# Optimization experiments

Measured on AMD Instinct MI355X. Metric: run time of the kernel, lower is better.

Reference implementation:

```python
import jax, jax.numpy as jnp
import numpy as np

N_HEAD = 8
EPS_LN = 1e-5
EPS_SM = 1e-16


def _mlp(x, w1, b1, g, beta, w2, b2):
    # Linear -> ReLU -> LayerNorm -> Linear (matches nn.Sequential in torch module)
    h = jax.nn.relu(x @ w1 + b1)
    mu = jnp.mean(h, axis=-1, keepdims=True)
    var = jnp.mean((h - mu) ** 2, axis=-1, keepdims=True)
    h = (h - mu) * jax.lax.rsqrt(var + EPS_LN) * g + beta
    return h @ w2 + b2


def setup_inputs() -> dict:
    B, L, D, E, Fe, H = 4, 4096, 128, 262144, 5, N_HEAD
    ks = jax.random.split(jax.random.key(0), 20)
    s = 0.02
    p = lambda i, sh: jax.random.normal(ks[i], sh, jnp.float32) * s
    z = lambda n: jnp.zeros((n,), jnp.float32)
    inp = {
        "key": jax.random.normal(ks[0], (B, L, D), jnp.float32),
        "value": jax.random.normal(ks[1], (B, L, D), jnp.float32),
        "query": jax.random.normal(ks[2], (B, L, D), jnp.float32),
        "edge_feats": jax.random.normal(ks[3], (E, Fe), jnp.float32),
        "atten_masks": jnp.zeros((E,), jnp.float32),  # present in signature, unused in forward
        "batch_indices": jax.random.randint(ks[4], (E,), 0, B),
        "head_indices": jax.random.randint(ks[5], (E,), 0, L),
        "tail_indices": jax.random.randint(ks[6], (E,), 0, L),
        "key_w": p(7, (D, D)), "key_b": z(D),
        "query_w": p(8, (D, D)), "query_b": z(D),
        "value_w": p(9, (D, D)), "value_b": z(D),
        "proj_w": p(10, (D, D)), "proj_b": z(D),
        "ea_w1": p(11, (Fe, D)), "ea_b1": z(D), "ea_g": jnp.ones((D,), jnp.float32), "ea_beta": z(D), "ea_w2": p(12, (D, H)), "ea_b2": z(H),
        "ek_w1": p(13, (Fe, D)), "ek_b1": z(D), "ek_g": jnp.ones((D,), jnp.float32), "ek_beta": z(D), "ek_w2": p(14, (D, D)), "ek_b2": z(D),
        "ev_w1": p(15, (Fe, D)), "ev_b1": z(D), "ev_g": jnp.ones((D,), jnp.float32), "ev_beta": z(D), "ev_w2": p(16, (D, D)), "ev_b2": z(D),
    }
    return inp


def reference(key, value, query, edge_feats, atten_masks,
              batch_indices, head_indices, tail_indices,
              key_w, key_b, query_w, query_b, value_w, value_b, proj_w, proj_b,
              ea_w1, ea_b1, ea_g, ea_beta, ea_w2, ea_b2,
              ek_w1, ek_b1, ek_g, ek_beta, ek_w2, ek_b2,
              ev_w1, ev_b1, ev_g, ev_beta, ev_w2, ev_b2):
    B, L, D = query.shape
    H = N_HEAD
    dh = D // H
    N = B * L
    # node projections -> [B*L, H, dh]
    k = (key @ key_w + key_b).reshape(N, H, dh)
    q = (query @ query_w + query_b).reshape(N, H, dh)
    v = (value @ value_w + value_b).reshape(N, H, dh)
    heads = batch_indices * L + head_indices  # destination node per edge
    tails = batch_indices * L + tail_indices  # source node per edge
    # per-edge gather + edge-conditioned k/v
    qs = q[heads]
    ks = k[tails] + _mlp(edge_feats, ek_w1, ek_b1, ek_g, ek_beta, ek_w2, ek_b2).reshape(-1, H, dh)
    vs = v[tails] + _mlp(edge_feats, ev_w1, ev_b1, ev_g, ev_beta, ev_w2, ev_b2).reshape(-1, H, dh)
    w = jnp.sum(ks * qs, axis=-1) + _mlp(edge_feats, ea_w1, ea_b1, ea_g, ea_beta, ea_w2, ea_b2)  # [E, H]
    # segment softmax over edges grouped by destination node
    m = jax.ops.segment_max(w, heads, num_segments=N)
    ex = jnp.exp(w - m[heads])
    denom = jax.ops.segment_sum(ex, heads, num_segments=N)
    att = ex / (denom[heads] + EPS_SM)  # [E, H]
    # weighted scatter-sum combine
    y = jax.ops.segment_sum(att[:, :, None] * vs, heads, num_segments=N).reshape(B, L, D)
    return y @ proj_w + proj_b
```

## Files before the change

### kernel.cpp

```cpp
#include <hip/hip_runtime.h>
#include <hip/hip_bf16.h>

#define D      128
#define NHEAD  8
#define FE     5
#define LSEQ   4096
#define EPB    64
#define NNODE  16384
#define EPS_LN 1e-5f
#define EPS_SM 1e-16f

typedef unsigned short ushort_t;
typedef __bf16 bf16x8 __attribute__((ext_vector_type(8)));
typedef float  f32x4  __attribute__((ext_vector_type(4)));

__device__ __forceinline__ ushort_t f2bf(float x) {
    __hip_bfloat16 b = __float2bfloat16(x);
    return __builtin_bit_cast(unsigned short, b);
}
__device__ __forceinline__ float bf2f(ushort_t u) {
    __hip_bfloat16 b = __builtin_bit_cast(__hip_bfloat16, u);
    return __bfloat162float(b);
}
__device__ __forceinline__ float i2f(int x)  { return __builtin_bit_cast(float, x); }
__device__ __forceinline__ int   f2i(float x){ return __builtin_bit_cast(int, x); }

union Pk8 { ushort_t u[8]; uint4 v; };

__global__ __launch_bounds__(256) void setup_kernel(
    const float* __restrict__ key, const float* __restrict__ value,
    const float* __restrict__ query,
    const float* __restrict__ key_w, const float* __restrict__ key_b,
    const float* __restrict__ value_w, const float* __restrict__ value_b,
    const float* __restrict__ query_w, const float* __restrict__ query_b,
    ushort_t* __restrict__ k16, ushort_t* __restrict__ v16, ushort_t* __restrict__ q16,
    const float* __restrict__ ekw2, const float* __restrict__ evw2,
    const float* __restrict__ eaw2,
    ushort_t* __restrict__ eksw, ushort_t* __restrict__ evsw, ushort_t* __restrict__ easw,
    const int* __restrict__ bidx, const int* __restrict__ hidx,
    int* __restrict__ cnt, int nqb, int E)
{
    const int t  = threadIdx.x;
    const int nq = 3 * nqb;

    if ((int)blockIdx.x < nq) {
        __shared__ float xs[2][D][20];
        const int which = blockIdx.x / nqb;
        const int r0    = (blockIdx.x % nqb) * 32;
        const float* X = (which == 0) ? key   : (which == 1) ? value   : query;
        const float* W = (which == 0) ? key_w : (which == 1) ? value_w : query_w;
        const float* bias = (which == 0) ? key_b : (which == 1) ? value_b : query_b;
        ushort_t* Y = (which == 0) ? k16 : (which == 1) ? v16 : q16;

        const int rg = t >> 7, j = t & 127;
        const int rbase = r0 + rg * 16;
        {
            float tmp[16];
            #pragma unroll
            for (int r = 0; r < 16; ++r) tmp[r] = X[(size_t)(rbase + r) * D + j];
            #pragma unroll
            for (int c = 0; c < 4; ++c)
                *(float4*)&xs[rg][j][c * 4] = float4{tmp[c*4], tmp[c*4+1], tmp[c*4+2], tmp[c*4+3]};
        }
        __syncthreads();
        float acc[16];
        const float b = bias[j];
        #pragma unroll
        for (int r = 0; r < 16; ++r) acc[r] = b;
        #pragma unroll 4
        for (int i = 0; i < D; ++i) {
            const float w = W[i * D + j];
            #pragma unroll
            for (int c = 0; c < 4; ++c) {
                const float4 x4 = *(const float4*)&xs[rg][i][c * 4];
                acc[c*4+0] = fmaf(x4.x, w, acc[c*4+0]);
                acc[c*4+1] = fmaf(x4.y, w, acc[c*4+1]);
                acc[c*4+2] = fmaf(x4.z, w, acc[c*4+2]);
                acc[c*4+3] = fmaf(x4.w, w, acc[c*4+3]);
            }
        }
        #pragma unroll
        for (int r = 0; r < 16; ++r) Y[(size_t)(rbase + r) * D + j] = f2bf(acc[r]);
        return;
    }

    const int b2 = blockIdx.x - nq;
    if (b2 < 17) {
        const int g = b2 * 256 + t;
        const float* src; ushort_t* dst; int frag, ncols, nvalid;
        if (g < 2048)      { src = ekw2; dst = eksw; frag = g;        ncols = 128; nvalid = 128; }
        else if (g < 4096) { src = evw2; dst = evsw; frag = g - 2048; ncols = 128; nvalid = 128; }
        else if (g < 4352) { src = eaw2; dst = easw; frag = g - 4096; ncols = 8;   nvalid = 8; }
        else return;
        const int s = (frag >> 6) & 3;
        const int l = frag & 63;
        const int n = ((frag >> 8) << 4) + (l & 15);
        Pk8 pk;
        #pragma unroll
        for (int j = 0; j < 8; ++j) {
            const int k = s * 32 + (l >> 4) * 8 + j;
            const float v = (n < nvalid) ? src[k * ncols + n] : 0.f;
            pk.u[j] = f2bf(v);
        }
        *(uint4*)(dst + (size_t)frag * 8) = pk.v;
        return;
    }

    const int e = (b2 - 17) * 256 + t;
    if (e < E) atomicAdd(&cnt[bidx[e] * LSEQ + hidx[e]], 1);
}

__global__ __launch_bounds__(1024) void scan16k(
    const int* __restrict__ cnt, int* __restrict__ base)
{
    __shared__ int part[1024];
    const int t = threadIdx.x;
    int v[16], ex[16], s = 0;
    #pragma unroll
    for (int i = 0; i < 16; ++i) v[i] = cnt[t * 16 + i];
    #pragma unroll
    for (int i = 0; i < 16; ++i) { ex[i] = s; s += v[i]; }
    part[t] = s;
    __syncthreads();
    for (int off = 1; off < 1024; off <<= 1) {
        const int x = (t >= off) ? part[t - off] : 0;
        __syncthreads();
        part[t] += x;
        __syncthreads();
    }
    const int boff = (t > 0) ? part[t - 1] : 0;
    #pragma unroll
    for (int i = 0; i < 16; ++i) base[t * 16 + i] = boff + ex[i];
    if (t == 1023) base[NNODE] = boff + s;
}

__global__ __launch_bounds__(256) void scatter_rec(
    const int* __restrict__ bidx, const int* __restrict__ hidx, const int* __restrict__ tidx,
    const float* __restrict__ edge_feats,
    const int* __restrict__ base, int* __restrict__ cnt,
    float* __restrict__ rec, int E)
{
    const int e = blockIdx.x * 256 + threadIdx.x;
    if (e >= E) return;
    const int bb = bidx[e];
    const int nh = bb * LSEQ + hidx[e];
    const int nt = bb * LSEQ + tidx[e];
    const int slot = atomicSub(&cnt[nh], 1) - 1;
    const int p = base[nh] + slot;
    float ef[FE];
    #pragma unroll
    for (int f = 0; f < FE; ++f) ef[f] = edge_feats[(size_t)e * FE + f];
    *(float4*)&rec[(size_t)p * 8]     = float4{ef[0], ef[1], ef[2], ef[3]};
    *(float4*)&rec[(size_t)p * 8 + 4] = float4{ef[4], i2f(nh), i2f(nt), 0.f};
}

__global__ __launch_bounds__(256, 4) void edge_kernel(
    const float* __restrict__ rec,
    const float* __restrict__ ea_w1, const float* __restrict__ ea_b1,
    const float* __restrict__ ea_g,  const float* __restrict__ ea_be, const float* __restrict__ ea_b2,
    const float* __restrict__ ek_w1, const float* __restrict__ ek_b1,
    const float* __restrict__ ek_g,  const float* __restrict__ ek_be, const float* __restrict__ ek_b2,
    const float* __restrict__ ev_w1, const float* __restrict__ ev_b1,
    const float* __restrict__ ev_g,  const float* __restrict__ ev_be, const float* __restrict__ ev_b2,
    const ushort_t* __restrict__ easw, const ushort_t* __restrict__ eksw, const ushort_t* __restrict__ evsw,
    const ushort_t* __restrict__ k16, const ushort_t* __restrict__ q16, const ushort_t* __restrict__ v16,
    float* __restrict__ ex_ws, ushort_t* __restrict__ vs_ws)
{
    __shared__ float pw1[3][FE * D];
    __shared__ float pb1[3][D], pg[3][D], pbe[3][D];
    __shared__ float pb2k[D], pb2v[D], pb2a[NHEAD];
    __shared__ float ef_s[EPB][FE];
    __shared__ int   eh_s[EPB], et_s[EPB];

    const int t   = threadIdx.x;
    const int e0g = blockIdx.x * EPB;

    for (int i = t; i < FE * D; i += 256) { pw1[0][i] = ea_w1[i]; pw1[1][i] = ek_w1[i]; pw1[2][i] = ev_w1[i]; }
    if (t < D) {
        pb1[0][t] = ea_b1[t]; pb1[1][t] = ek_b1[t]; pb1[2][t] = ev_b1[t];
        pg [0][t] = ea_g [t]; pg [1][t] = ek_g [t]; pg [2][t] = ev_g [t];
        pbe[0][t] = ea_be[t]; pbe[1][t] = ek_be[t]; pbe[2][t] = ev_be[t];
        pb2k[t] = ek_b2[t];   pb2v[t] = ev_b2[t];
        if (t < NHEAD) pb2a[t] = ea_b2[t];
    }
    if (t < 128) {
        const int pl = t >> 1, half = t & 1;
        const float4 v = *(const float4*)&rec[((size_t)e0g + pl) * 8 + half * 4];
        if (half == 0) {
            ef_s[pl][0] = v.x; ef_s[pl][1] = v.y; ef_s[pl][2] = v.z; ef_s[pl][3] = v.w;
        } else {
            ef_s[pl][4] = v.x; eh_s[pl] = f2i(v.y); et_s[pl] = f2i(v.z);
        }
    }
    __syncthreads();

    const int mt   = t >> 6;
    const int l    = t & 63;
    const int qt   = l & 3;
    const int per  = l >> 2;
    const int row0 = (l >> 4) * 4;
    const int colb = l & 15;
    const int src  = 4 * colb + (l >> 4);
    const int bsrc = (l & 48);

    int tn[4], hnn[4];
    #pragma unroll
    for (int r = 0; r < 4; ++r) { tn[r] = et_s[mt*16 + row0 + r]; hnn[r] = eh_s[mt*16 + row0 + r]; }

    float efr[FE];
    #pragma unroll
    for (int f = 0; f < FE; ++f) efr[f] = ef_s[mt*16 + per][f];

    auto first_layer = [&](int m, uint4 pk[4]) {
        const float4* w1v = (const float4*)&pw1[m][0];
        const float4* b1v = (const float4*)&pb1[m][0];
        const float4* gv  = (const float4*)&pg[m][0];
        const float4* bev = (const float4*)&pbe[m][0];
        float4 hv[4][2];
        float s1 = 0.f, s2 = 0.f;
        #pragma unroll
        for (int s = 0; s < 4; ++s) {
            #pragma unroll
            for (int hc = 0; hc < 2; ++hc) {
                const int idx = s * 8 + qt * 2 + hc;
                float4 a = b1v[idx];
                #pragma unroll
                for (int f = 0; f < FE; ++f) {
                    const float sc = efr[f];
                    const float4 w = w1v[f * 32 + idx];
                    a.x = fmaf(sc, w.x, a.x); a.y = fmaf(sc, w.y, a.y);
                    a.z = fmaf(sc, w.z, a.z); a.w = fmaf(sc, w.w, a.w);
                }
                a.x = fmaxf(a.x, 0.f); a.y = fmaxf(a.y, 0.f);
                a.z = fmaxf(a.z, 0.f); a.w = fmaxf(a.w, 0.f);
                hv[s][hc] = a;
                s1 += a.x + a.y + a.z + a.w;
                s2 += a.x*a.x + a.y*a.y + a.z*a.z + a.w*a.w;
            }
        }
        s1 += __shfl_xor(s1, 1); s1 += __shfl_xor(s1, 2);
        s2 += __shfl_xor(s2, 1); s2 += __shfl_xor(s2, 2);
        const float mu = s1 * (1.f / 128.f);
        const float rs = rsqrtf(s2 * (1.f / 128.f) - mu * mu + EPS_LN);
        #pragma unroll
        for (int s = 0; s < 4; ++s) {
            const int idx = s * 8 + qt * 2;
            const float4 x0 = hv[s][0], x1 = hv[s][1];
            const float4 g0 = gv[idx], g1 = gv[idx + 1];
            const float4 b0 = bev[idx], b1 = bev[idx + 1];
            Pk8 p8;
            p8.u[0] = f2bf(fmaf((x0.x - mu) * rs, g0.x, b0.x));
            p8.u[1] = f2bf(fmaf((x0.y - mu) * rs, g0.y, b0.y));
            p8.u[2] = f2bf(fmaf((x0.z - mu) * rs, g0.z, b0.z));
            p8.u[3] = f2bf(fmaf((x0.w - mu) * rs, g0.w, b0.w));
            p8.u[4] = f2bf(fmaf((x1.x - mu) * rs, g1.x, b1.x));
            p8.u[5] = f2bf(fmaf((x1.y - mu) * rs, g1.y, b1.y));
            p8.u[6] = f2bf(fmaf((x1.z - mu) * rs, g1.z, b1.z));
            p8.u[7] = f2bf(fmaf((x1.w - mu) * rs, g1.w, b1.w));
            pk[s] = p8.v;
        }
    };

    auto gather_afr = [&](const uint4 pk[4], bf16x8 afr[4]) {
        #pragma unroll
        for (int s = 0; s < 4; ++s) {
            uint4 w;
            w.x = (unsigned)__shfl((int)pk[s].x, src);
            w.y = (unsigned)__shfl((int)pk[s].y, src);
            w.z = (unsigned)__shfl((int)pk[s].z, src);
            w.w = (unsigned)__shfl((int)pk[s].w, src);
            afr[s] = __builtin_bit_cast(bf16x8, w);
        }
    };

    uint4 pk[4];
    bf16x8 afr[4];

    float eaacc[4];
    first_layer(0, pk);
    gather_afr(pk, afr);
    {
        f32x4 acc = {0.f, 0.f, 0.f, 0.f};
        #pragma unroll
        for (int s = 0; s < 4; ++s) {
            const bf16x8 bfr = *(const bf16x8*)(easw + (size_t)(s * 64 + l) * 8);
            acc = __builtin_amdgcn_mfma_f32_16x16x32_bf16(afr[s], bfr, acc, 0, 0, 0);
        }
        #pragma unroll
        for (int r = 0; r < 4; ++r) eaacc[r] = acc[r];
    }

    first_layer(1, pk);
    gather_afr(pk, afr);
    #pragma unroll
    for (int nt = 0; nt < NHEAD; ++nt) {
        f32x4 acc = {0.f, 0.f, 0.f, 0.f};
        #pragma unroll
        for (int s = 0; s < 4; ++s) {
            const bf16x8 bfr = *(const bf16x8*)(eksw + (size_t)((nt * 4 + s) * 64 + l) * 8);
            acc = __builtin_amdgcn_mfma_f32_16x16x32_bf16(afr[s], bfr, acc, 0, 0, 0);
        }
        const int col = nt * 16 + colb;
        const float b2 = pb2k[col];
        const float ba = pb2a[nt];
        float pr[4];
        #pragma unroll
        for (int r = 0; r < 4; ++r)
            pr[r] = (acc[r] + b2 + bf2f(k16[(size_t)tn[r] * D + col]))
                    * bf2f(q16[(size_t)hnn[r] * D + col]);
        #pragma unroll
        for (int m = 1; m < 16; m <<= 1) {
            #pragma unroll
            for (int r = 0; r < 4; ++r) pr[r] += __shfl_xor(pr[r], m);
        }
        #pragma unroll
        for (int r = 0; r < 4; ++r) {
            const float ea = __shfl(eaacc[r], bsrc | nt);
            const float ex = __expf(pr[r] + ea + ba);
            if (colb == nt)
                ex_ws[(size_t)(e0g + mt*16 + row0 + r) * NHEAD + nt] = ex;
        }
    }

    first_layer(2, pk);
    gather_afr(pk, afr);
    #pragma unroll
    for (int nt = 0; nt < NHEAD; ++nt) {
        f32x4 acc = {0.f, 0.f, 0.f, 0.f};
        #pragma unroll
        for (int s = 0; s < 4; ++s) {
            const bf16x8 bfr = *(const bf16x8*)(evsw + (size_t)((nt * 4 + s) * 64 + l) * 8);
            acc = __builtin_amdgcn_mfma_f32_16x16x32_bf16(afr[s], bfr, acc, 0, 0, 0);
        }
        const int col = nt * 16 + colb;
        const float b2 = pb2v[col];
        #pragma unroll
        for (int r = 0; r < 4; ++r) {
            const float vs = acc[r] + b2 + bf2f(v16[(size_t)tn[r] * D + col]);
            vs_ws[(size_t)(e0g + mt*16 + row0 + r) * D + col] = f2bf(vs);
        }
    }
}

__global__ __launch_bounds__(512) void agg_out(
    const int* __restrict__ base,
    const float* __restrict__ ex_ws, const ushort_t* __restrict__ vs_ws,
    const float* __restrict__ W, const float* __restrict__ bias,
    float* __restrict__ out)
{
    __shared__ float xs[D][20];
    const int t  = threadIdx.x;
    const int rg = t >> 7;
    const int j  = t & 127;
    const int h  = j >> 4;
    const int n0 = blockIdx.x * 16;

    #pragma unroll
    for (int ni = 0; ni < 4; ++ni) {
        const int n  = n0 + rg * 4 + ni;
        const int s0 = base[n], s1 = base[n + 1];
        float acc = 0.f, den = 0.f;
        int p = s0;
        for (; p + 4 <= s1; p += 4) {
            float ex4[4], vs4[4];
            #pragma unroll
            for (int r = 0; r < 4; ++r) {
                ex4[r] = ex_ws[(size_t)(p + r) * NHEAD + h];
                vs4[r] = bf2f(vs_ws[(size_t)(p + r) * D + j]);
            }
            #pragma unroll
            for (int r = 0; r < 4; ++r) {
                den += ex4[r];
                acc = fmaf(ex4[r], vs4[r], acc);
            }
        }
        for (; p < s1; ++p) {
            const float ex = ex_ws[(size_t)p * NHEAD + h];
            den += ex;
            acc = fmaf(ex, bf2f(vs_ws[(size_t)p * D + j]), acc);
        }
        xs[j][rg * 4 + ni] = acc / (den + EPS_SM);
    }
    __syncthreads();

    float acc[4];
    const float b = bias[j];
    #pragma unroll
    for (int r = 0; r < 4; ++r) acc[r] = b;
    #pragma unroll 4
    for (int i = 0; i < D; ++i) {
        const float w = W[i * D + j];
        const float4 y4 = *(const float4*)&xs[i][rg * 4];
        acc[0] = fmaf(y4.x, w, acc[0]); acc[1] = fmaf(y4.y, w, acc[1]);
        acc[2] = fmaf(y4.z, w, acc[2]); acc[3] = fmaf(y4.w, w, acc[3]);
    }
    #pragma unroll
    for (int r = 0; r < 4; ++r)
        out[(size_t)(n0 + rg * 4 + r) * D + j] = acc[r];
}

extern "C" void kernel_launch(void* const* d_in, const int* in_sizes, int n_in,
                              void* d_out, int out_size, void* d_ws, size_t ws_size,
                              hipStream_t stream)
{
    const float* key        = (const float*)d_in[0];
    const float* value      = (const float*)d_in[1];
    const float* query      = (const float*)d_in[2];
    const float* edge_feats = (const float*)d_in[3];
    const int*   bidx       = (const int*)d_in[5];
    const int*   hidx       = (const int*)d_in[6];
    const int*   tidx       = (const int*)d_in[7];
    const float* key_w   = (const float*)d_in[8];  const float* key_b   = (const float*)d_in[9];
    const float* query_w = (const float*)d_in[10]; const float* query_b = (const float*)d_in[11];
    const float* value_w = (const float*)d_in[12]; const float* value_b = (const float*)d_in[13];
    const float* proj_w  = (const float*)d_in[14]; const float* proj_b  = (const float*)d_in[15];

    const int N = in_sizes[0] / D;
    const int E = in_sizes[5];

    char* ws = (char*)d_ws;
    ushort_t* k16   = (ushort_t*)ws; ws += (size_t)N * D * 2;
    ushort_t* q16   = (ushort_t*)ws; ws += (size_t)N * D * 2;
    ushort_t* v16   = (ushort_t*)ws; ws += (size_t)N * D * 2;
    float* ex_ws    = (float*)ws;    ws += (size_t)E * NHEAD * 4;
    ushort_t* vs_ws = (ushort_t*)ws; ws += (size_t)E * D * 2;
    float* rec      = (float*)ws;    ws += (size_t)E * 8 * 4;
    ushort_t* eksw  = (ushort_t*)ws; ws += (size_t)2048 * 8 * 2;
    ushort_t* evsw  = (ushort_t*)ws; ws += (size_t)2048 * 8 * 2;
    ushort_t* easw  = (ushort_t*)ws; ws += (size_t)256 * 8 * 2;
    int* base = (int*)ws;  ws += (size_t)(N + 1) * 4;
    int* cnt  = (int*)ws;  ws += (size_t)N * 4;

    const int nqb   = N / 32;
    const int nhist = (E + 255) / 256;
    const int ngrid = 3 * nqb + 17 + nhist;

    hipMemsetAsync(cnt, 0, (size_t)N * 4, stream);

    setup_kernel<<<ngrid, 256, 0, stream>>>(
        key, value, query,
        key_w, key_b, value_w, value_b, query_w, query_b,
        k16, v16, q16,
        (const float*)d_in[26], (const float*)d_in[32], (const float*)d_in[20],
        eksw, evsw, easw,
        bidx, hidx, cnt, nqb, E);

    scan16k<<<1, 1024, 0, stream>>>(cnt, base);

    scatter_rec<<<(E + 255) / 256, 256, 0, stream>>>(
        bidx, hidx, tidx, edge_feats, base, cnt, rec, E);

    edge_kernel<<<E / EPB, 256, 0, stream>>>(
        rec,
        (const float*)d_in[16], (const float*)d_in[17], (const float*)d_in[18],
        (const float*)d_in[19], (const float*)d_in[21],
        (const float*)d_in[22], (const float*)d_in[23], (const float*)d_in[24],
        (const float*)d_in[25], (const float*)d_in[27],
        (const float*)d_in[28], (const float*)d_in[29], (const float*)d_in[30],
        (const float*)d_in[31], (const float*)d_in[33],
        easw, eksw, evsw,
        k16, q16, v16,
        ex_ws, vs_ws);

    agg_out<<<N / 16, 512, 0, stream>>>(base, ex_ws, vs_ws, proj_w, proj_b, (float*)d_out);
}
```

Measured before the change: 311.4 us.

## Move K/Q/V projections to bf16 MFMA and merge them with edge scatter kernel

The fp32 FMA node projections for key/query/value are replaced by bf16 MFMA 16x16x32 tiles. Their weights are pre-swizzled into fragment layout in the pre-kernel, next to the edge MLP weights. The projection blocks move into the same launch as the edge record scatter, so the projections overlap with the scatter work and the histogram/scan runs before them. This cuts fp32 ALU cost, but inputs are now rounded to bf16 before the matmul, which lowers precision.

Result: faster. 293.5 us (-5.7%).

```diff
diff --git a/kernel.cpp b/kernel.cpp
--- a/kernel.cpp
+++ b/kernel.cpp
@@ -27,70 +27,26 @@
 
 union Pk8 { ushort_t u[8]; uint4 v; };
 
-__global__ __launch_bounds__(256) void setup_kernel(
-    const float* __restrict__ key, const float* __restrict__ value,
-    const float* __restrict__ query,
-    const float* __restrict__ key_w, const float* __restrict__ key_b,
-    const float* __restrict__ value_w, const float* __restrict__ value_b,
-    const float* __restrict__ query_w, const float* __restrict__ query_b,
-    ushort_t* __restrict__ k16, ushort_t* __restrict__ v16, ushort_t* __restrict__ q16,
+__global__ __launch_bounds__(256) void pre_kernel(
     const float* __restrict__ ekw2, const float* __restrict__ evw2,
     const float* __restrict__ eaw2,
+    const float* __restrict__ kw, const float* __restrict__ qw,
+    const float* __restrict__ vw,
     ushort_t* __restrict__ eksw, ushort_t* __restrict__ evsw, ushort_t* __restrict__ easw,
+    ushort_t* __restrict__ kwsw, ushort_t* __restrict__ qwsw, ushort_t* __restrict__ vwsw,
     const int* __restrict__ bidx, const int* __restrict__ hidx,
-    int* __restrict__ cnt, int nqb, int E)
-{
-    const int t  = threadIdx.x;
-    const int nq = 3 * nqb;
-
-    if ((int)blockIdx.x < nq) {
-        __shared__ float xs[2][D][20];
-        const int which = blockIdx.x / nqb;
-        const int r0    = (blockIdx.x % nqb) * 32;
-        const float* X = (which == 0) ? key   : (which == 1) ? value   : query;
-        const float* W = (which == 0) ? key_w : (which == 1) ? value_w : query_w;
-        const float* bias = (which == 0) ? key_b : (which == 1) ? value_b : query_b;
-        ushort_t* Y = (which == 0) ? k16 : (which == 1) ? v16 : q16;
-
-        const int rg = t >> 7, j = t & 127;
-        const int rbase = r0 + rg * 16;
-        {
-            float tmp[16];
-            #pragma unroll
-            for (int r = 0; r < 16; ++r) tmp[r] = X[(size_t)(rbase + r) * D + j];
-            #pragma unroll
-            for (int c = 0; c < 4; ++c)
-                *(float4*)&xs[rg][j][c * 4] = float4{tmp[c*4], tmp[c*4+1], tmp[c*4+2], tmp[c*4+3]};
-        }
-        __syncthreads();
-        float acc[16];
-        const float b = bias[j];
-        #pragma unroll
-        for (int r = 0; r < 16; ++r) acc[r] = b;
-        #pragma unroll 4
-        for (int i = 0; i < D; ++i) {
-            const float w = W[i * D + j];
-            #pragma unroll
-            for (int c = 0; c < 4; ++c) {
-                const float4 x4 = *(const float4*)&xs[rg][i][c * 4];
-                acc[c*4+0] = fmaf(x4.x, w, acc[c*4+0]);
-                acc[c*4+1] = fmaf(x4.y, w, acc[c*4+1]);
-                acc[c*4+2] = fmaf(x4.z, w, acc[c*4+2]);
-                acc[c*4+3] = fmaf(x4.w, w, acc[c*4+3]);
-            }
-        }
-        #pragma unroll
-        for (int r = 0; r < 16; ++r) Y[(size_t)(rbase + r) * D + j] = f2bf(acc[r]);
-        return;
-    }
-
-    const int b2 = blockIdx.x - nq;
-    if (b2 < 17) {
-        const int g = b2 * 256 + t;
-        const float* src; ushort_t* dst; int frag, ncols, nvalid;
-        if (g < 2048)      { src = ekw2; dst = eksw; frag = g;        ncols = 128; nvalid = 128; }
-        else if (g < 4096) { src = evw2; dst = evsw; frag = g - 2048; ncols = 128; nvalid = 128; }
-        else if (g < 4352) { src = eaw2; dst = easw; frag = g - 4096; ncols = 8;   nvalid = 8; }
+    int* __restrict__ cnt, int E)
+{
+    const int t = threadIdx.x;
+    if (blockIdx.x < 41) {
+        const int g = blockIdx.x * 256 + t;
+        const float* src; ushort_t* dst; int frag, ncols = 128, nvalid = 128;
+        if (g < 2048)       { src = ekw2; dst = eksw; frag = g; }
+        else if (g < 4096)  { src = evw2; dst = evsw; frag = g - 2048; }
+        else if (g < 4352)  { src = eaw2; dst = easw; frag = g - 4096; ncols = 8; nvalid = 8; }
+        else if (g < 6400)  { src = kw;   dst = kwsw; frag = g - 4352; }
+        else if (g < 8448)  { src = qw;   dst = qwsw; frag = g - 6400; }
+        else if (g < 10496) { src = vw;   dst = vwsw; frag = g - 8448; }
         else return;
         const int s = (frag >> 6) & 3;
         const int l = frag & 63;
@@ -105,8 +61,7 @@
         *(uint4*)(dst + (size_t)frag * 8) = pk.v;
         return;
     }
-
-    const int e = (b2 - 17) * 256 + t;
+    const int e = (blockIdx.x - 41) * 256 + t;
     if (e < E) atomicAdd(&cnt[bidx[e] * LSEQ + hidx[e]], 1);
 }
 
@@ -134,13 +89,67 @@
     if (t == 1023) base[NNODE] = boff + s;
 }
 
-__global__ __launch_bounds__(256) void scatter_rec(
+__global__ __launch_bounds__(256) void mid_kernel(
+    const float* __restrict__ key, const float* __restrict__ value,
+    const float* __restrict__ query,
+    const float* __restrict__ key_b, const float* __restrict__ value_b,
+    const float* __restrict__ query_b,
+    const ushort_t* __restrict__ kwsw, const ushort_t* __restrict__ vwsw,
+    const ushort_t* __restrict__ qwsw,
+    ushort_t* __restrict__ k16, ushort_t* __restrict__ v16, ushort_t* __restrict__ q16,
     const int* __restrict__ bidx, const int* __restrict__ hidx, const int* __restrict__ tidx,
     const float* __restrict__ edge_feats,
-    const int* __restrict__ base, int* __restrict__ cnt,
-    float* __restrict__ rec, int E)
-{
-    const int e = blockIdx.x * 256 + threadIdx.x;
+    const int* __restrict__ base, int* __restrict__ cnt, float* __restrict__ rec,
+    int nqm, int E)
+{
+    const int t  = threadIdx.x;
+    const int nq = 3 * nqm;
+    if ((int)blockIdx.x < nq) {
+        const int which = blockIdx.x / nqm;
+        const int blk   = blockIdx.x % nqm;
+        const float* X     = (which == 0) ? key   : (which == 1) ? value   : query;
+        const float* bias  = (which == 0) ? key_b : (which == 1) ? value_b : query_b;
+        const ushort_t* Ww = (which == 0) ? kwsw  : (which == 1) ? vwsw    : qwsw;
+        ushort_t* Y        = (which == 0) ? k16   : (which == 1) ? v16     : q16;
+
+        const int mt    = t >> 6;
+        const int l     = t & 63;
+        const int rbase = blk * 64 + mt * 16;
+        const int colb  = l & 15;
+        const int row0  = (l >> 4) * 4;
+        const int arow  = rbase + colb;
+        const int koff  = (l >> 4) * 8;
+
+        bf16x8 afr[4];
+        #pragma unroll
+        for (int s = 0; s < 4; ++s) {
+            const float4 x0 = *(const float4*)&X[(size_t)arow * D + s * 32 + koff];
+            const float4 x1 = *(const float4*)&X[(size_t)arow * D + s * 32 + koff + 4];
+            Pk8 p8;
+            p8.u[0] = f2bf(x0.x); p8.u[1] = f2bf(x0.y);
+            p8.u[2] = f2bf(x0.z); p8.u[3] = f2bf(x0.w);
+            p8.u[4] = f2bf(x1.x); p8.u[5] = f2bf(x1.y);
+            p8.u[6] = f2bf(x1.z); p8.u[7] = f2bf(x1.w);
+            afr[s] = __builtin_bit_cast(bf16x8, p8.v);
+        }
+        #pragma unroll
+        for (int nt = 0; nt < 8; ++nt) {
+            f32x4 acc = {0.f, 0.f, 0.f, 0.f};
+            #pragma unroll
+            for (int s = 0; s < 4; ++s) {
+                const bf16x8 bfr = *(const bf16x8*)(Ww + (size_t)((nt * 4 + s) * 64 + l) * 8);
+                acc = __builtin_amdgcn_mfma_f32_16x16x32_bf16(afr[s], bfr, acc, 0, 0, 0);
+            }
+            const int col = nt * 16 + colb;
+            const float b = bias[col];
+            #pragma unroll
+            for (int r = 0; r < 4; ++r)
+                Y[(size_t)(rbase + row0 + r) * D + col] = f2bf(acc[r] + b);
+        }
+        return;
+    }
+
+    const int e = (blockIdx.x - nq) * 256 + t;
     if (e >= E) return;
     const int bb = bidx[e];
     const int nh = bb * LSEQ + hidx[e];
@@ -428,27 +437,32 @@
     ushort_t* eksw  = (ushort_t*)ws; ws += (size_t)2048 * 8 * 2;
     ushort_t* evsw  = (ushort_t*)ws; ws += (size_t)2048 * 8 * 2;
     ushort_t* easw  = (ushort_t*)ws; ws += (size_t)256 * 8 * 2;
+    ushort_t* kwsw  = (ushort_t*)ws; ws += (size_t)2048 * 8 * 2;
+    ushort_t* qwsw  = (ushort_t*)ws; ws += (size_t)2048 * 8 * 2;
+    ushort_t* vwsw  = (ushort_t*)ws; ws += (size_t)2048 * 8 * 2;
     int* base = (int*)ws;  ws += (size_t)(N + 1) * 4;
     int* cnt  = (int*)ws;  ws += (size_t)N * 4;
 
-    const int nqb   = N / 32;
+    const int nqm   = N / 64;
     const int nhist = (E + 255) / 256;
-    const int ngrid = 3 * nqb + 17 + nhist;
 
     hipMemsetAsync(cnt, 0, (size_t)N * 4, stream);
 
-    setup_kernel<<<ngrid, 256, 0, stream>>>(
+    pre_kernel<<<41 + nhist, 256, 0, stream>>>(
+        (const float*)d_in[26], (const float*)d_in[32], (const float*)d_in[20],
+        key_w, query_w, value_w,
+        eksw, evsw, easw, kwsw, qwsw, vwsw,
+        bidx, hidx, cnt, E);
+
+    scan16k<<<1, 1024, 0, stream>>>(cnt, base);
+
+    mid_kernel<<<3 * nqm + nhist, 256, 0, stream>>>(
         key, value, query,
-        key_w, key_b, value_w, value_b, query_w, query_b,
+        key_b, value_b, query_b,
+        kwsw, vwsw, qwsw,
         k16, v16, q16,
-        (const float*)d_in[26], (const float*)d_in[32], (const float*)d_in[20],
-        eksw, evsw, easw,
-        bidx, hidx, cnt, nqb, E);
-
-    scan16k<<<1, 1024, 0, stream>>>(cnt, base);
-
-    scatter_rec<<<(E + 255) / 256, 256, 0, stream>>>(
-        bidx, hidx, tidx, edge_feats, base, cnt, rec, E);
+        bidx, hidx, tidx, edge_feats,
+        base, cnt, rec, nqm, E);
 
     edge_kernel<<<E / EPB, 256, 0, stream>>>(
         rec,
```
